# Performance work log

Measured on AMD Instinct MI355X. Metric: run time of the kernel, lower is better.

The kernel has to match this reference:

```python
import jax, jax.numpy as jnp
import numpy as np

B, T, D = 4, 4096, 1024
E, C, O = 8, 1024, 512  # experts, capacity per expert, per-expert out features


def setup_inputs() -> dict:
    key = jax.random.key(0)
    k1, k2, k3, k4 = jax.random.split(key, 4)
    x = jax.random.normal(k1, (B, T, D), dtype=jnp.float32)
    expert_indices = jax.random.randint(k2, (B, E, C), 0, T)
    # nn.Linear(in, out) weight is (out, in) = (E*O, D); reshape -> (E, O, D)
    bound = 1.0 / np.sqrt(D)
    weight = jax.random.uniform(k3, (E, O, D), dtype=jnp.float32, minval=-bound, maxval=bound)
    bias = jax.random.uniform(k4, (E, O), dtype=jnp.float32, minval=-bound, maxval=bound)
    return {"x": x, "expert_indices": expert_indices, "weight": weight, "bias": bias}


def reference(x, expert_indices, weight, bias):
    # gather_experts: select C tokens per (batch, expert) -> (B, E, C, D)
    b_idx = jnp.arange(x.shape[0])[:, None, None]
    selected = x[b_idx, expert_indices]  # (B, E, C, D)
    # per-expert grouped GEMM + bias
    out = jnp.einsum('becd,eod->beco', selected, weight)
    out = out + bias[None, :, None, :]
    return out
```

## Files before the change

kernel.cpp:

```cpp
#include <hip/hip_runtime.h>
#include <stdint.h>

#define Bdim 4
#define Tdim 4096
#define Ddim 1024
#define Edim 8
#define Cdim 1024
#define Odim 512

using bf16x8 = __attribute__((ext_vector_type(8))) __bf16;
using f32x4  = __attribute__((ext_vector_type(4))) float;

__device__ __forceinline__ unsigned short f2bf(float f) {
  unsigned int u = __float_as_uint(f);
  u += 0x7fffu + ((u >> 16) & 1u);
  return (unsigned short)(u >> 16);
}

__global__ void cast_f32_to_bf16(const float* __restrict__ xin,
                                 const float* __restrict__ win,
                                 unsigned short* __restrict__ outp,
                                 int nx4, int ntot4) {
  int i = blockIdx.x * blockDim.x + threadIdx.x;
  if (i >= ntot4) return;
  float4 v;
  if (i < nx4) v = reinterpret_cast<const float4*>(xin)[i];
  else         v = reinterpret_cast<const float4*>(win)[i - nx4];
  ushort4 o;
  o.x = f2bf(v.x); o.y = f2bf(v.y); o.z = f2bf(v.z); o.w = f2bf(v.w);
  reinterpret_cast<ushort4*>(outp)[i] = o;
}

__device__ __forceinline__ void async_copy16(const unsigned short* g,
                                             unsigned short* l) {
  __builtin_amdgcn_global_load_lds(
      (__attribute__((address_space(1))) unsigned int*)g,
      (__attribute__((address_space(3))) unsigned int*)l, 16, 0, 0);
}

__global__ __launch_bounds__(256) void moe_mfma_gemm(
    const unsigned short* __restrict__ xbf,
    const unsigned short* __restrict__ wbf,
    const int* __restrict__ idx,
    const float* __restrict__ bias,
    float* __restrict__ out) {
  __shared__ __align__(16) unsigned short sA[2][128 * 64];
  __shared__ __align__(16) unsigned short sB[2][128 * 64];
  __shared__ int sTok[128];

  const int bid = blockIdx.x;
  const int be = bid >> 5;
  const int mt = (bid >> 2) & 7;
  const int nt = bid & 3;
  const int b = be >> 3;
  const int e = be & 7;

  const int tid = threadIdx.x;
  const int lane = tid & 63;
  const int wid = tid >> 6;
  const int wm = wid >> 1;
  const int wn = wid & 1;

  if (tid < 128) sTok[tid] = idx[be * Cdim + mt * 128 + tid];
  __syncthreads();

  const int rsub = lane >> 3;
  const int kcol = (((lane & 7) ^ rsub) * 8);
  const unsigned short* gA[4];
  const unsigned short* gB[4];
#pragma unroll
  for (int i = 0; i < 4; ++i) {
    const int r = wid * 32 + i * 8 + rsub;
    gA[i] = xbf + ((size_t)(b * Tdim + sTok[r])) * Ddim + kcol;
    gB[i] = wbf + ((size_t)(e * Odim + nt * 128 + r)) * Ddim + kcol;
  }
  const int ldsRowOff = (wid * 32) * 64;

  f32x4 acc[4][4];
#pragma unroll
  for (int im = 0; im < 4; ++im)
#pragma unroll
    for (int in = 0; in < 4; ++in) acc[im][in] = (f32x4){0.f, 0.f, 0.f, 0.f};

  const int fr = lane & 15;
  const int fkc = lane >> 4;
  const int sw = fr & 7;

#pragma unroll
  for (int i = 0; i < 4; ++i) {
    async_copy16(gA[i], &sA[0][ldsRowOff + i * 8 * 64]);
    async_copy16(gB[i], &sB[0][ldsRowOff + i * 8 * 64]);
  }

#pragma unroll
  for (int k0 = 0; k0 < 16; ++k0) {
    const int cur = k0 & 1;
    __syncthreads();
    if (k0 < 15) {
      const int koff = (k0 + 1) * 64;
#pragma unroll
      for (int i = 0; i < 4; ++i) {
        async_copy16(gA[i] + koff, &sA[cur ^ 1][ldsRowOff + i * 8 * 64]);
        async_copy16(gB[i] + koff, &sB[cur ^ 1][ldsRowOff + i * 8 * 64]);
      }
    }
#pragma unroll
    for (int kb = 0; kb < 2; ++kb) {
      const int ko = ((kb * 4 + fkc) ^ sw) * 8;
      bf16x8 af[4], bfr[4];
#pragma unroll
      for (int im = 0; im < 4; ++im)
        af[im] = *(const bf16x8*)&sA[cur][(size_t)(wm * 64 + im * 16 + fr) * 64 + ko];
#pragma unroll
      for (int in = 0; in < 4; ++in)
        bfr[in] = *(const bf16x8*)&sB[cur][(size_t)(wn * 64 + in * 16 + fr) * 64 + ko];
#pragma unroll
      for (int im = 0; im < 4; ++im)
#pragma unroll
        for (int in = 0; in < 4; ++in)
          acc[im][in] = __builtin_amdgcn_mfma_f32_16x16x32_bf16(
              af[im], bfr[in], acc[im][in], 0, 0, 0);
    }
  }

  float bv[4];
#pragma unroll
  for (int in = 0; in < 4; ++in)
    bv[in] = bias[e * Odim + nt * 128 + wn * 64 + in * 16 + fr];

  const int crow0 = (lane >> 4) * 4;
  float* outBase = out + (size_t)be * (Cdim * Odim) + (size_t)(mt * 128) * Odim + nt * 128;
#pragma unroll
  for (int im = 0; im < 4; ++im) {
    float* pr = outBase + (size_t)(wm * 64 + im * 16 + crow0) * Odim;
#pragma unroll
    for (int in = 0; in < 4; ++in) {
      float* p = pr + wn * 64 + in * 16 + fr;
#pragma unroll
      for (int r = 0; r < 4; ++r) p[(size_t)r * Odim] = acc[im][in][r] + bv[in];
    }
  }
}

extern "C" void kernel_launch(void* const* d_in, const int* in_sizes, int n_in,
                              void* d_out, int out_size, void* d_ws, size_t ws_size,
                              hipStream_t stream) {
  const float* x = (const float*)d_in[0];
  const int* idx = (const int*)d_in[1];
  const float* w = (const float*)d_in[2];
  const float* bias = (const float*)d_in[3];
  float* out = (float*)d_out;

  unsigned short* xbf = (unsigned short*)d_ws;
  unsigned short* wbf = xbf + (size_t)Bdim * Tdim * Ddim;

  const int nx4 = Bdim * Tdim * Ddim / 4;
  const int ntot4 = nx4 + Edim * Odim * Ddim / 4;
  cast_f32_to_bf16<<<(ntot4 + 255) / 256, 256, 0, stream>>>(x, w, xbf, nx4, ntot4);

  moe_mfma_gemm<<<1024, 256, 0, stream>>>(xbf, wbf, idx, bias, out);
}
```

Before: 175.7 us.

## Load gathered A fragments directly from global into registers, drop A LDS staging

Removes the shared-memory buffer for the gathered token rows. Each lane now loads its MFMA A-fragments straight from global memory into registers and prefetches them one K-step ahead, while B stays double-buffered in LDS. This cuts LDS traffic and halves LDS usage, which may allow more resident blocks. The cost is that each wave reads A rows redundantly across the two wn waves, using less coalesced 16-byte global loads, and register pressure rises from the prefetch buffers.

```diff
diff --git a/kernel.cpp b/kernel.cpp
--- a/kernel.cpp
+++ b/kernel.cpp
@@ -44,7 +44,6 @@
     const int* __restrict__ idx,
     const float* __restrict__ bias,
     float* __restrict__ out) {
-  __shared__ __align__(16) unsigned short sA[2][128 * 64];
   __shared__ __align__(16) unsigned short sB[2][128 * 64];
   __shared__ int sTok[128];
 
@@ -64,17 +63,26 @@
   if (tid < 128) sTok[tid] = idx[be * Cdim + mt * 128 + tid];
   __syncthreads();
 
+  const int fr = lane & 15;
+  const int fkc = lane >> 4;
+  const int sw = fr & 7;
+
+  const unsigned short* gAf[4];
+#pragma unroll
+  for (int im = 0; im < 4; ++im) {
+    const int row = wm * 64 + im * 16 + fr;
+    gAf[im] = xbf + ((size_t)(b * Tdim + sTok[row])) * Ddim + fkc * 8;
+  }
+
   const int rsub = lane >> 3;
   const int kcol = (((lane & 7) ^ rsub) * 8);
-  const unsigned short* gA[4];
   const unsigned short* gB[4];
 #pragma unroll
   for (int i = 0; i < 4; ++i) {
     const int r = wid * 32 + i * 8 + rsub;
-    gA[i] = xbf + ((size_t)(b * Tdim + sTok[r])) * Ddim + kcol;
     gB[i] = wbf + ((size_t)(e * Odim + nt * 128 + r)) * Ddim + kcol;
   }
-  const int ldsRowOff = (wid * 32) * 64;
+  const int ldsOff = (wid * 32) * 64;
 
   f32x4 acc[4][4];
 #pragma unroll
@@ -82,35 +90,47 @@
 #pragma unroll
     for (int in = 0; in < 4; ++in) acc[im][in] = (f32x4){0.f, 0.f, 0.f, 0.f};
 
-  const int fr = lane & 15;
-  const int fkc = lane >> 4;
-  const int sw = fr & 7;
+#pragma unroll
+  for (int i = 0; i < 4; ++i) async_copy16(gB[i], &sB[0][ldsOff + i * 8 * 64]);
 
+  bf16x8 afN[2][4];
 #pragma unroll
-  for (int i = 0; i < 4; ++i) {
-    async_copy16(gA[i], &sA[0][ldsRowOff + i * 8 * 64]);
-    async_copy16(gB[i], &sB[0][ldsRowOff + i * 8 * 64]);
-  }
+  for (int kb = 0; kb < 2; ++kb)
+#pragma unroll
+    for (int im = 0; im < 4; ++im)
+      afN[kb][im] = *(const bf16x8*)(gAf[im] + kb * 32);
 
 #pragma unroll
   for (int k0 = 0; k0 < 16; ++k0) {
     const int cur = k0 & 1;
     __syncthreads();
+
     if (k0 < 15) {
       const int koff = (k0 + 1) * 64;
 #pragma unroll
-      for (int i = 0; i < 4; ++i) {
-        async_copy16(gA[i] + koff, &sA[cur ^ 1][ldsRowOff + i * 8 * 64]);
-        async_copy16(gB[i] + koff, &sB[cur ^ 1][ldsRowOff + i * 8 * 64]);
-      }
+      for (int i = 0; i < 4; ++i)
+        async_copy16(gB[i] + koff, &sB[cur ^ 1][ldsOff + i * 8 * 64]);
     }
+
+    bf16x8 afC[2][4];
+#pragma unroll
+    for (int kb = 0; kb < 2; ++kb)
+#pragma unroll
+      for (int im = 0; im < 4; ++im) afC[kb][im] = afN[kb][im];
+
+    if (k0 < 15) {
+      const int koff = (k0 + 1) * 64;
+#pragma unroll
+      for (int kb = 0; kb < 2; ++kb)
+#pragma unroll
+        for (int im = 0; im < 4; ++im)
+          afN[kb][im] = *(const bf16x8*)(gAf[im] + koff + kb * 32);
+    }
+
 #pragma unroll
     for (int kb = 0; kb < 2; ++kb) {
       const int ko = ((kb * 4 + fkc) ^ sw) * 8;
-      bf16x8 af[4], bfr[4];
-#pragma unroll
-      for (int im = 0; im < 4; ++im)
-        af[im] = *(const bf16x8*)&sA[cur][(size_t)(wm * 64 + im * 16 + fr) * 64 + ko];
+      bf16x8 bfr[4];
 #pragma unroll
       for (int in = 0; in < 4; ++in)
         bfr[in] = *(const bf16x8*)&sB[cur][(size_t)(wn * 64 + in * 16 + fr) * 64 + ko];
@@ -119,7 +139,7 @@
 #pragma unroll
         for (int in = 0; in < 4; ++in)
           acc[im][in] = __builtin_amdgcn_mfma_f32_16x16x32_bf16(
-              af[im], bfr[in], acc[im][in], 0, 0, 0);
+              afC[kb][im], bfr[in], acc[im][in], 0, 0, 0);
     }
   }
 
```

After: 208.4 us. 18.6% more time.
